# Kernel optimization log

Hardware: AMD Instinct MI355X
Metric: run time of the kernel (lower is better)

## Reference

```python
import jax, jax.numpy as jnp
import numpy as np

C = 32          # in_channels = out_channels = groups
K = 3           # kernel_size
STRIDE = 2
PAD = 1
DIL = 1
EPS = 1e-20


def _depthwise_convT(x, w):
    """Equivalent of torch.F.conv_transpose2d(x, w, groups=C, stride=STRIDE,
    padding=PAD, dilation=DIL) with w of shape (C, 1, K, K).
    Implemented as an lhs-dilated conv with a spatially flipped kernel."""
    w_f = w[:, :, ::-1, ::-1]
    pad = DIL * (K - 1) - PAD  # = 1 for K=3, PAD=1, DIL=1
    return jax.lax.conv_general_dilated(
        x, w_f,
        window_strides=(1, 1),
        padding=[(pad, pad), (pad, pad)],
        lhs_dilation=(STRIDE, STRIDE),
        rhs_dilation=(DIL, DIL),
        dimension_numbers=('NCHW', 'OIHW', 'NCHW'),
        feature_group_count=C)


def setup_inputs() -> dict:
    key = jax.random.key(0)
    k = jax.random.split(key, 7)
    B, H, W = 2, 176, 608
    # depths/confidences are positive (rand); gy is signed (randn)
    d = jax.random.uniform(k[0], (B, C, H, W), dtype=jnp.float32) + 0.5
    cd = jax.random.uniform(k[1], (B, C, H, W), dtype=jnp.float32)
    gy = jax.random.normal(k[2], (B, C, H, W), dtype=jnp.float32)
    cgy = jax.random.uniform(k[3], (B, C, H, W), dtype=jnp.float32)
    w_prop_raw = jax.random.normal(k[4], (1, C, 1, 1), dtype=jnp.float32)
    spatial_weight_raw = jax.random.normal(k[5], (C, 1, K, K), dtype=jnp.float32)
    bias = 0.01 * jax.random.normal(k[6], (1, C, 1, 1), dtype=jnp.float32)
    return {"d": d, "cd": cd, "gy": gy, "cgy": cgy,
            "w_prop_raw": w_prop_raw,
            "spatial_weight_raw": spatial_weight_raw,
            "bias": bias}


def reference(d, cd, gy, cgy, w_prop_raw, spatial_weight_raw, bias):
    # EnforcePos('softplus') on both learned weights
    w_prop = jax.nn.softplus(w_prop_raw)          # (1, C, 1, 1)
    sw = jax.nn.softplus(spatial_weight_raw)      # (C, 1, K, K)

    # roll-based vertical neighbor gather with edge confidence zeroing
    d_up = jnp.roll(d, 1, axis=2)
    cd_up = jnp.roll(cd, 1, axis=2).at[:, :, 0, :].set(0.0)
    d_down = jnp.roll(d, -1, axis=2)
    cd_down = jnp.roll(cd, -1, axis=2).at[:, :, -1, :].set(0.0)

    cgy_from_ds = cd_up * cd_up
    height = (cd_up * d_up + cd_down * d_down) / (cd_up + cd_down)
    gy_from_ds = (d_down - d_up) / 2.0 / height

    gy_f = (w_prop * cgy * gy + cgy_from_ds * gy_from_ds) / (w_prop * cgy + cgy_from_ds)
    cgy_f = (w_prop * cgy + cgy_from_ds) / (w_prop + 1.0)

    nom = _depthwise_convT(cgy_f * gy_f, sw)
    denom = _depthwise_convT(cgy_f, sw)
    cdenom = _depthwise_convT(jnp.ones_like(cgy_f), sw)

    # original adds bias twice: once unconditionally, once under use_bias
    gy_out = nom / (denom + EPS) + bias + bias
    cgy_out = denom / (cdenom + EPS)
    return gy_out / STRIDE, cgy_out
```

## Files before the change

kernel.cpp:

```cpp
#include <hip/hip_runtime.h>
#include <math.h>

#define B_   2
#define C_   32
#define H_   176
#define W_   608
#define HO_  351
#define WO_  1215
#define PLANE_O (HO_ * WO_)
#define OUT1_O  (B_ * C_ * PLANE_O)
#define EPS_ 1e-20f
#define NTH  512
#define W4   (W_ / 4)
#define HW_  304

typedef float f4_t __attribute__((ext_vector_type(4)));
typedef float f2_t __attribute__((ext_vector_type(2)));

__device__ __forceinline__ float softplus_f(float x) {
    return fmaxf(x, 0.0f) + log1pf(expf(-fabsf(x)));
}

extern "C" __global__ __launch_bounds__(NTH, 8)
void structn_rows(const float* __restrict__ d,
                  const float* __restrict__ cd,
                  const float* __restrict__ gy,
                  const float* __restrict__ cgy,
                  const float* __restrict__ wpr,
                  const float* __restrict__ swr,
                  const float* __restrict__ bias,
                  float* __restrict__ out)
{
    __shared__ float s_nE[5 * HW_];
    __shared__ float s_nO[5 * HW_];
    __shared__ float s_cE[5 * HW_];
    __shared__ float s_cO[5 * HW_];

    const int g     = blockIdx.x;
    const int plane = blockIdx.y;
    const int c     = plane & (C_ - 1);

    float sw[9];
#pragma unroll
    for (int k = 0; k < 9; ++k) sw[k] = softplus_f(swr[c * 9 + k]);
    const float wp      = softplus_f(wpr[c]);
    const float inv_wp1 = 1.0f / (wp + 1.0f);
    const float bv      = bias[c];
    const float icd_ee  = 1.0f / (sw[4] + EPS_);
    const float icd_eo  = 1.0f / (sw[3] + sw[5] + EPS_);
    const float icd_oe  = 1.0f / (sw[1] + sw[7] + EPS_);
    const float icd_oo  = 1.0f / (sw[0] + sw[2] + sw[6] + sw[8] + EPS_);

    const int r0  = g * 4;
    const int nrf = (r0 + 4 <= H_ - 1) ? 5 : (H_ - r0);

    const int pbase = plane * (H_ * W_);
    const float* __restrict__ dP  = d   + pbase;
    const float* __restrict__ cdP = cd  + pbase;
    const float* __restrict__ gyP = gy  + pbase;
    const float* __restrict__ cgP = cgy + pbase;

    const int ntask = nrf * W4;
    for (int idx = threadIdx.x; idx < ntask; idx += NTH) {
        const int rf = idx / W4;
        const int iw = (idx - rf * W4) << 2;
        const int iy = r0 + rf;
        const int up = (iy == 0)      ? (H_ - 1) : iy - 1;
        const int dn = (iy == H_ - 1) ? 0        : iy + 1;
        const float mu = (iy > 0)      ? 1.0f : 0.0f;
        const float md = (iy < H_ - 1) ? 1.0f : 0.0f;

        const f4_t du = *(const f4_t*)(dP  + up * W_ + iw);
        const f4_t dd = *(const f4_t*)(dP  + dn * W_ + iw);
        const f4_t cu = *(const f4_t*)(cdP + up * W_ + iw);
        const f4_t cn = *(const f4_t*)(cdP + dn * W_ + iw);
        const f4_t gg = *(const f4_t*)(gyP + iy * W_ + iw);
        const f4_t cg = *(const f4_t*)(cgP + iy * W_ + iw);

        f4_t sn4, sc4;
#pragma unroll
        for (int e = 0; e < 4; ++e) {
            const float cuv = cu[e] * mu;
            const float cnv = cn[e] * md;
            const float cfd = cuv * cuv;
            const float rs  = __builtin_amdgcn_rcpf(fmaf(cuv, du[e], cnv * dd[e]));
            const float gfd = 0.5f * (dd[e] - du[e]) * (cuv + cnv) * rs;
            const float num = fmaf(wp * cg[e], gg[e], cfd * gfd);
            const float den = fmaf(wp, cg[e], cfd);
            sn4[e] = num * inv_wp1;
            sc4[e] = den * inv_wp1;
        }
        const int eo = rf * HW_ + (iw >> 1);
        f2_t v;
        v[0] = sn4[0]; v[1] = sn4[2];  *(f2_t*)(s_nE + eo) = v;
        v[0] = sn4[1]; v[1] = sn4[3];  *(f2_t*)(s_nO + eo) = v;
        v[0] = sc4[0]; v[1] = sc4[2];  *(f2_t*)(s_cE + eo) = v;
        v[0] = sc4[1]; v[1] = sc4[3];  *(f2_t*)(s_cO + eo) = v;
    }
    __syncthreads();

    const int w    = threadIdx.x >> 6;
    const int lane = threadIdx.x & 63;
    const int oy   = g * 8 + w;
    if (oy >= HO_) return;

    const int p   = w & 1;
    const int lrA = w >> 1;

    const int ro0 = plane * PLANE_O + oy * WO_;
    float* __restrict__ o0 = out + ro0;
    float* __restrict__ o1 = out + OUT1_O + ro0;

    const int h  = (4 - (ro0 & 3)) & 3;
    const int n4 = (WO_ - h) >> 2;
    const int q  = h & 1;
    const int r  = (h >> 1) & 1;

    const float icdC = p ? icd_oe : icd_ee;
    const float icdO = p ? icd_oo : icd_eo;
    const float i0 = q ? icdO : icdC;
    const float i1 = q ? icdC : icdO;

    const float* __restrict__ nAE = s_nE + lrA * HW_;
    const float* __restrict__ nAO = s_nO + lrA * HW_;
    const float* __restrict__ cAE = s_cE + lrA * HW_;
    const float* __restrict__ cAO = s_cO + lrA * HW_;

#define VAL(E, O, j) (((j) & 1) ? (O)[((j) - 1) >> 1] : (E)[(j) >> 1])

    if (p == 0) {
        if (lane < 3) {
            const int ox = (lane < h) ? lane : (h + (n4 << 2) + lane - h);
            float den, nom, icd;
            if ((ox & 1) == 0) {
                const int j = ox >> 1;
                den = VAL(cAE, cAO, j) * sw[4];
                nom = VAL(nAE, nAO, j) * sw[4];
                icd = icd_ee;
            } else {
                const int j = (ox - 1) >> 1;
                den = VAL(cAE, cAO, j) * sw[5] + VAL(cAE, cAO, j + 1) * sw[3];
                nom = VAL(nAE, nAO, j) * sw[5] + VAL(nAE, nAO, j + 1) * sw[3];
                icd = icd_eo;
            }
            o0[ox] = fmaf(0.5f * nom, __builtin_amdgcn_rcpf(den + EPS_), bv);
            o1[ox] = den * icd;
        }
        const float* pa0 = r ? nAO : nAE;
        const float* pa1 = r ? nAE + 1 : nAO;
        const float* pa2 = r ? nAO + 1 : nAE + 1;
        const float* px0 = r ? cAO : cAE;
        const float* px1 = r ? cAE + 1 : cAO;
        const float* px2 = r ? cAO + 1 : cAE + 1;

        for (int k = lane; k < n4; k += 64) {
            const float a0 = pa0[k], a1 = pa1[k], a2 = pa2[k];
            const float x0 = px0[k], x1 = px1[k], x2 = px2[k];
            const float dC0 = x0 * sw[4], dC1 = x1 * sw[4], dC2 = x2 * sw[4];
            const float nC0 = a0 * sw[4], nC1 = a1 * sw[4], nC2 = a2 * sw[4];
            const float dF0 = x0 * sw[5] + x1 * sw[3];
            const float dF1 = x1 * sw[5] + x2 * sw[3];
            const float nF0 = a0 * sw[5] + a1 * sw[3];
            const float nF1 = a1 * sw[5] + a2 * sw[3];

            const float d0 = q ? dF0 : dC0, n0 = q ? nF0 : nC0;
            const float d1 = q ? dC1 : dF0, n1 = q ? nC1 : nF0;
            const float d2 = q ? dF1 : dC1, n2 = q ? nF1 : nC1;
            const float d3 = q ? dC2 : dF1, n3 = q ? nC2 : nF1;

            f4_t gv, qv;
            gv[0] = fmaf(0.5f * n0, __builtin_amdgcn_rcpf(d0 + EPS_), bv);
            gv[1] = fmaf(0.5f * n1, __builtin_amdgcn_rcpf(d1 + EPS_), bv);
            gv[2] = fmaf(0.5f * n2, __builtin_amdgcn_rcpf(d2 + EPS_), bv);
            gv[3] = fmaf(0.5f * n3, __builtin_amdgcn_rcpf(d3 + EPS_), bv);
            qv[0] = d0 * i0; qv[1] = d1 * i1; qv[2] = d2 * i0; qv[3] = d3 * i1;

            const int c0 = h + (k << 2);
            __builtin_nontemporal_store(gv, (f4_t*)(o0 + c0));
            __builtin_nontemporal_store(qv, (f4_t*)(o1 + c0));
        }
    } else {
        const float* __restrict__ nBE = nAE + HW_;
        const float* __restrict__ nBO = nAO + HW_;
        const float* __restrict__ cBE = cAE + HW_;
        const float* __restrict__ cBO = cAO + HW_;

        if (lane < 3) {
            const int ox = (lane < h) ? lane : (h + (n4 << 2) + lane - h);
            float den, nom, icd;
            if ((ox & 1) == 0) {
                const int j = ox >> 1;
                den = VAL(cAE, cAO, j) * sw[7] + VAL(cBE, cBO, j) * sw[1];
                nom = VAL(nAE, nAO, j) * sw[7] + VAL(nBE, nBO, j) * sw[1];
                icd = icd_oe;
            } else {
                const int j = (ox - 1) >> 1;
                den = VAL(cAE, cAO, j) * sw[8] + VAL(cAE, cAO, j + 1) * sw[6]
                    + VAL(cBE, cBO, j) * sw[2] + VAL(cBE, cBO, j + 1) * sw[0];
                nom = VAL(nAE, nAO, j) * sw[8] + VAL(nAE, nAO, j + 1) * sw[6]
                    + VAL(nBE, nBO, j) * sw[2] + VAL(nBE, nBO, j + 1) * sw[0];
                icd = icd_oo;
            }
            o0[ox] = fmaf(0.5f * nom, __builtin_amdgcn_rcpf(den + EPS_), bv);
            o1[ox] = den * icd;
        }

        const float* pa0 = r ? nAO : nAE;
        const float* pa1 = r ? nAE + 1 : nAO;
        const float* pa2 = r ? nAO + 1 : nAE + 1;
        const float* px0 = r ? cAO : cAE;
        const float* px1 = r ? cAE + 1 : cAO;
        const float* px2 = r ? cAO + 1 : cAE + 1;
        const float* pb0 = r ? nBO : nBE;
        const float* pb1 = r ? nBE + 1 : nBO;
        const float* pb2 = r ? nBO + 1 : nBE + 1;
        const float* py0 = r ? cBO : cBE;
        const float* py1 = r ? cBE + 1 : cBO;
        const float* py2 = r ? cBO + 1 : cBE + 1;

        for (int k = lane; k < n4; k += 64) {
            const float a0 = pa0[k], a1 = pa1[k], a2 = pa2[k];
            const float x0 = px0[k], x1 = px1[k], x2 = px2[k];
            const float b0 = pb0[k], b1 = pb1[k], b2 = pb2[k];
            const float y0 = py0[k], y1 = py1[k], y2 = py2[k];

            const float dC0 = x0 * sw[7] + y0 * sw[1];
            const float dC1 = x1 * sw[7] + y1 * sw[1];
            const float dC2 = x2 * sw[7] + y2 * sw[1];
            const float nC0 = a0 * sw[7] + b0 * sw[1];
            const float nC1 = a1 * sw[7] + b1 * sw[1];
            const float nC2 = a2 * sw[7] + b2 * sw[1];
            const float dF0 = x0 * sw[8] + x1 * sw[6] + y0 * sw[2] + y1 * sw[0];
            const float dF1 = x1 * sw[8] + x2 * sw[6] + y1 * sw[2] + y2 * sw[0];
            const float nF0 = a0 * sw[8] + a1 * sw[6] + b0 * sw[2] + b1 * sw[0];
            const float nF1 = a1 * sw[8] + a2 * sw[6] + b1 * sw[2] + b2 * sw[0];

            const float d0 = q ? dF0 : dC0, n0 = q ? nF0 : nC0;
            const float d1 = q ? dC1 : dF0, n1 = q ? nC1 : nF0;
            const float d2 = q ? dF1 : dC1, n2 = q ? nF1 : nC1;
            const float d3 = q ? dC2 : dF1, n3 = q ? nC2 : nF1;

            f4_t gv, qv;
            gv[0] = fmaf(0.5f * n0, __builtin_amdgcn_rcpf(d0 + EPS_), bv);
            gv[1] = fmaf(0.5f * n1, __builtin_amdgcn_rcpf(d1 + EPS_), bv);
            gv[2] = fmaf(0.5f * n2, __builtin_amdgcn_rcpf(d2 + EPS_), bv);
            gv[3] = fmaf(0.5f * n3, __builtin_amdgcn_rcpf(d3 + EPS_), bv);
            qv[0] = d0 * i0; qv[1] = d1 * i1; qv[2] = d2 * i0; qv[3] = d3 * i1;

            const int c0 = h + (k << 2);
            __builtin_nontemporal_store(gv, (f4_t*)(o0 + c0));
            __builtin_nontemporal_store(qv, (f4_t*)(o1 + c0));
        }
    }
#undef VAL
}

extern "C" void kernel_launch(void* const* d_in, const int* in_sizes, int n_in,
                              void* d_out, int out_size, void* d_ws, size_t ws_size,
                              hipStream_t stream) {
    const float* d    = (const float*)d_in[0];
    const float* cd   = (const float*)d_in[1];
    const float* gy   = (const float*)d_in[2];
    const float* cgy  = (const float*)d_in[3];
    const float* wpr  = (const float*)d_in[4];
    const float* swr  = (const float*)d_in[5];
    const float* bias = (const float*)d_in[6];
    float* out = (float*)d_out;

    dim3 grid(44, B_ * C_);
    structn_rows<<<grid, NTH, 0, stream>>>(d, cd, gy, cgy, wpr, swr, bias, out);
}
```

Measured before the change: 73.81 us.

## Process two row-groups per block, overlapping second staging with first output half

Each block now covers 16 output rows (8 input rows plus halo) instead of 8, with shared memory sized for 9 input rows. Staging of rows 5..8 is issued before the first half of outputs is computed, so global loads can overlap LDS reads and stores, and the shared halo row is loaded once instead of twice. The grid is halved and the occupancy hint drops from 8 to 6 blocks because of the larger LDS footprint, which cuts available parallelism.

```diff
diff --git a/kernel.cpp b/kernel.cpp
--- a/kernel.cpp
+++ b/kernel.cpp
@@ -13,6 +13,7 @@
 #define NTH  512
 #define W4   (W_ / 4)
 #define HW_  304
+#define NRLDS 9
 
 typedef float f4_t __attribute__((ext_vector_type(4)));
 typedef float f2_t __attribute__((ext_vector_type(2)));
@@ -21,8 +22,8 @@
     return fmaxf(x, 0.0f) + log1pf(expf(-fabsf(x)));
 }
 
-extern "C" __global__ __launch_bounds__(NTH, 8)
-void structn_rows(const float* __restrict__ d,
+extern "C" __global__ __launch_bounds__(NTH, 6)
+void structn_pipe(const float* __restrict__ d,
                   const float* __restrict__ cd,
                   const float* __restrict__ gy,
                   const float* __restrict__ cgy,
@@ -31,12 +32,12 @@
                   const float* __restrict__ bias,
                   float* __restrict__ out)
 {
-    __shared__ float s_nE[5 * HW_];
-    __shared__ float s_nO[5 * HW_];
-    __shared__ float s_cE[5 * HW_];
-    __shared__ float s_cO[5 * HW_];
-
-    const int g     = blockIdx.x;
+    __shared__ float s_nE[NRLDS * HW_];
+    __shared__ float s_nO[NRLDS * HW_];
+    __shared__ float s_cE[NRLDS * HW_];
+    __shared__ float s_cO[NRLDS * HW_];
+
+    const int G     = blockIdx.x;
     const int plane = blockIdx.y;
     const int c     = plane & (C_ - 1);
 
@@ -51,8 +52,7 @@
     const float icd_oe  = 1.0f / (sw[1] + sw[7] + EPS_);
     const float icd_oo  = 1.0f / (sw[0] + sw[2] + sw[6] + sw[8] + EPS_);
 
-    const int r0  = g * 4;
-    const int nrf = (r0 + 4 <= H_ - 1) ? 5 : (H_ - r0);
+    const int f0 = G * 8;
 
     const int pbase = plane * (H_ * W_);
     const float* __restrict__ dP  = d   + pbase;
@@ -60,199 +60,209 @@
     const float* __restrict__ gyP = gy  + pbase;
     const float* __restrict__ cgP = cgy + pbase;
 
-    const int ntask = nrf * W4;
-    for (int idx = threadIdx.x; idx < ntask; idx += NTH) {
-        const int rf = idx / W4;
-        const int iw = (idx - rf * W4) << 2;
-        const int iy = r0 + rf;
-        const int up = (iy == 0)      ? (H_ - 1) : iy - 1;
-        const int dn = (iy == H_ - 1) ? 0        : iy + 1;
-        const float mu = (iy > 0)      ? 1.0f : 0.0f;
-        const float md = (iy < H_ - 1) ? 1.0f : 0.0f;
-
-        const f4_t du = *(const f4_t*)(dP  + up * W_ + iw);
-        const f4_t dd = *(const f4_t*)(dP  + dn * W_ + iw);
-        const f4_t cu = *(const f4_t*)(cdP + up * W_ + iw);
-        const f4_t cn = *(const f4_t*)(cdP + dn * W_ + iw);
-        const f4_t gg = *(const f4_t*)(gyP + iy * W_ + iw);
-        const f4_t cg = *(const f4_t*)(cgP + iy * W_ + iw);
-
-        f4_t sn4, sc4;
+    auto stage_rows = [&](int j0, int j1) {
+        const int ntask = (j1 - j0) * W4;
+        for (int idx = threadIdx.x; idx < ntask; idx += NTH) {
+            const int rf = j0 + idx / W4;
+            const int iw = (idx - (rf - j0) * W4) << 2;
+            const int iy = f0 + rf;
+            const int up = (iy == 0)      ? (H_ - 1) : iy - 1;
+            const int dn = (iy == H_ - 1) ? 0        : iy + 1;
+            const float mu = (iy > 0)      ? 1.0f : 0.0f;
+            const float md = (iy < H_ - 1) ? 1.0f : 0.0f;
+
+            const f4_t du = *(const f4_t*)(dP  + up * W_ + iw);
+            const f4_t dd = *(const f4_t*)(dP  + dn * W_ + iw);
+            const f4_t cu = *(const f4_t*)(cdP + up * W_ + iw);
+            const f4_t cn = *(const f4_t*)(cdP + dn * W_ + iw);
+            const f4_t gg = *(const f4_t*)(gyP + iy * W_ + iw);
+            const f4_t cg = *(const f4_t*)(cgP + iy * W_ + iw);
+
+            f4_t sn4, sc4;
 #pragma unroll
-        for (int e = 0; e < 4; ++e) {
-            const float cuv = cu[e] * mu;
-            const float cnv = cn[e] * md;
-            const float cfd = cuv * cuv;
-            const float rs  = __builtin_amdgcn_rcpf(fmaf(cuv, du[e], cnv * dd[e]));
-            const float gfd = 0.5f * (dd[e] - du[e]) * (cuv + cnv) * rs;
-            const float num = fmaf(wp * cg[e], gg[e], cfd * gfd);
-            const float den = fmaf(wp, cg[e], cfd);
-            sn4[e] = num * inv_wp1;
-            sc4[e] = den * inv_wp1;
+            for (int e = 0; e < 4; ++e) {
+                const float cuv = cu[e] * mu;
+                const float cnv = cn[e] * md;
+                const float cfd = cuv * cuv;
+                const float rs  = __builtin_amdgcn_rcpf(fmaf(cuv, du[e], cnv * dd[e]));
+                const float gfd = 0.5f * (dd[e] - du[e]) * (cuv + cnv) * rs;
+                const float num = fmaf(wp * cg[e], gg[e], cfd * gfd);
+                const float den = fmaf(wp, cg[e], cfd);
+                sn4[e] = num * inv_wp1;
+                sc4[e] = den * inv_wp1;
+            }
+            const int eo = rf * HW_ + (iw >> 1);
+            f2_t v;
+            v[0] = sn4[0]; v[1] = sn4[2];  *(f2_t*)(s_nE + eo) = v;
+            v[0] = sn4[1]; v[1] = sn4[3];  *(f2_t*)(s_nO + eo) = v;
+            v[0] = sc4[0]; v[1] = sc4[2];  *(f2_t*)(s_cE + eo) = v;
+            v[0] = sc4[1]; v[1] = sc4[3];  *(f2_t*)(s_cO + eo) = v;
         }
-        const int eo = rf * HW_ + (iw >> 1);
-        f2_t v;
-        v[0] = sn4[0]; v[1] = sn4[2];  *(f2_t*)(s_nE + eo) = v;
-        v[0] = sn4[1]; v[1] = sn4[3];  *(f2_t*)(s_nO + eo) = v;
-        v[0] = sc4[0]; v[1] = sc4[2];  *(f2_t*)(s_cE + eo) = v;
-        v[0] = sc4[1]; v[1] = sc4[3];  *(f2_t*)(s_cO + eo) = v;
-    }
-    __syncthreads();
+    };
 
     const int w    = threadIdx.x >> 6;
     const int lane = threadIdx.x & 63;
-    const int oy   = g * 8 + w;
-    if (oy >= HO_) return;
-
-    const int p   = w & 1;
-    const int lrA = w >> 1;
-
-    const int ro0 = plane * PLANE_O + oy * WO_;
-    float* __restrict__ o0 = out + ro0;
-    float* __restrict__ o1 = out + OUT1_O + ro0;
-
-    const int h  = (4 - (ro0 & 3)) & 3;
-    const int n4 = (WO_ - h) >> 2;
-    const int q  = h & 1;
-    const int r  = (h >> 1) & 1;
-
-    const float icdC = p ? icd_oe : icd_ee;
-    const float icdO = p ? icd_oo : icd_eo;
-    const float i0 = q ? icdO : icdC;
-    const float i1 = q ? icdC : icdO;
-
-    const float* __restrict__ nAE = s_nE + lrA * HW_;
-    const float* __restrict__ nAO = s_nO + lrA * HW_;
-    const float* __restrict__ cAE = s_cE + lrA * HW_;
-    const float* __restrict__ cAO = s_cO + lrA * HW_;
+
+    auto consume_half = [&](int h) {
+        const int oy = G * 16 + 8 * h + w;
+        if (oy >= HO_) return;
+
+        const int p   = w & 1;
+        const int lrA = 4 * h + (w >> 1);
+
+        const int ro0 = plane * PLANE_O + oy * WO_;
+        float* __restrict__ o0 = out + ro0;
+        float* __restrict__ o1 = out + OUT1_O + ro0;
+
+        const int h4 = (4 - (ro0 & 3)) & 3;
+        const int n4 = (WO_ - h4) >> 2;
+        const int q  = h4 & 1;
+        const int r  = (h4 >> 1) & 1;
+
+        const float icdC = p ? icd_oe : icd_ee;
+        const float icdO = p ? icd_oo : icd_eo;
+        const float i0 = q ? icdO : icdC;
+        const float i1 = q ? icdC : icdO;
+
+        const float* __restrict__ nAE = s_nE + lrA * HW_;
+        const float* __restrict__ nAO = s_nO + lrA * HW_;
+        const float* __restrict__ cAE = s_cE + lrA * HW_;
+        const float* __restrict__ cAO = s_cO + lrA * HW_;
 
 #define VAL(E, O, j) (((j) & 1) ? (O)[((j) - 1) >> 1] : (E)[(j) >> 1])
-
-    if (p == 0) {
-        if (lane < 3) {
-            const int ox = (lane < h) ? lane : (h + (n4 << 2) + lane - h);
-            float den, nom, icd;
-            if ((ox & 1) == 0) {
-                const int j = ox >> 1;
-                den = VAL(cAE, cAO, j) * sw[4];
-                nom = VAL(nAE, nAO, j) * sw[4];
-                icd = icd_ee;
-            } else {
-                const int j = (ox - 1) >> 1;
-                den = VAL(cAE, cAO, j) * sw[5] + VAL(cAE, cAO, j + 1) * sw[3];
-                nom = VAL(nAE, nAO, j) * sw[5] + VAL(nAE, nAO, j + 1) * sw[3];
-                icd = icd_eo;
-            }
-            o0[ox] = fmaf(0.5f * nom, __builtin_amdgcn_rcpf(den + EPS_), bv);
-            o1[ox] = den * icd;
+        if (p == 0) {
+            if (lane < 3) {
+                const int ox = (lane < h4) ? lane : (h4 + (n4 << 2) + lane - h4);
+                float den, nom, icd;
+                if ((ox & 1) == 0) {
+                    const int j = ox >> 1;
+                    den = VAL(cAE, cAO, j) * sw[4];
+                    nom = VAL(nAE, nAO, j) * sw[4];
+                    icd = icd_ee;
+                } else {
+                    const int j = (ox - 1) >> 1;
+                    den = VAL(cAE, cAO, j) * sw[5] + VAL(cAE, cAO, j + 1) * sw[3];
+                    nom = VAL(nAE, nAO, j) * sw[5] + VAL(nAE, nAO, j + 1) * sw[3];
+                    icd = icd_eo;
+                }
+                o0[ox] = fmaf(0.5f * nom, __builtin_amdgcn_rcpf(den + EPS_), bv);
+                o1[ox] = den * icd;
+            }
+            const float* pa0 = r ? nAO : nAE;
+            const float* pa1 = r ? nAE + 1 : nAO;
+            const float* pa2 = r ? nAO + 1 : nAE + 1;
+            const float* px0 = r ? cAO : cAE;
+            const float* px1 = r ? cAE + 1 : cAO;
+            const float* px2 = r ? cAO + 1 : cAE + 1;
+
+            for (int k = lane; k < n4; k += 64) {
+                const float a0 = pa0[k], a1 = pa1[k], a2 = pa2[k];
+                const float x0 = px0[k], x1 = px1[k], x2 = px2[k];
+                const float dC0 = x0 * sw[4], dC1 = x1 * sw[4], dC2 = x2 * sw[4];
+                const float nC0 = a0 * sw[4], nC1 = a1 * sw[4], nC2 = a2 * sw[4];
+                const float dF0 = x0 * sw[5] + x1 * sw[3];
+                const float dF1 = x1 * sw[5] + x2 * sw[3];
+                const float nF0 = a0 * sw[5] + a1 * sw[3];
+                const float nF1 = a1 * sw[5] + a2 * sw[3];
+
+                const float d0 = q ? dF0 : dC0, n0 = q ? nF0 : nC0;
+                const float d1 = q ? dC1 : dF0, n1 = q ? nC1 : nF0;
+                const float d2 = q ? dF1 : dC1, n2 = q ? nF1 : nC1;
+                const float d3 = q ? dC2 : dF1, n3 = q ? nC2 : nF1;
+
+                f4_t gv, qv;
+                gv[0] = fmaf(0.5f * n0, __builtin_amdgcn_rcpf(d0 + EPS_), bv);
+                gv[1] = fmaf(0.5f * n1, __builtin_amdgcn_rcpf(d1 + EPS_), bv);
+                gv[2] = fmaf(0.5f * n2, __builtin_amdgcn_rcpf(d2 + EPS_), bv);
+                gv[3] = fmaf(0.5f * n3, __builtin_amdgcn_rcpf(d3 + EPS_), bv);
+                qv[0] = d0 * i0; qv[1] = d1 * i1; qv[2] = d2 * i0; qv[3] = d3 * i1;
+
+                const int c0 = h4 + (k << 2);
+                __builtin_nontemporal_store(gv, (f4_t*)(o0 + c0));
+                __builtin_nontemporal_store(qv, (f4_t*)(o1 + c0));
+            }
+        } else {
+            const float* __restrict__ nBE = nAE + HW_;
+            const float* __restrict__ nBO = nAO + HW_;
+            const float* __restrict__ cBE = cAE + HW_;
+            const float* __restrict__ cBO = cAO + HW_;
+
+            if (lane < 3) {
+                const int ox = (lane < h4) ? lane : (h4 + (n4 << 2) + lane - h4);
+                float den, nom, icd;
+                if ((ox & 1) == 0) {
+                    const int j = ox >> 1;
+                    den = VAL(cAE, cAO, j) * sw[7] + VAL(cBE, cBO, j) * sw[1];
+                    nom = VAL(nAE, nAO, j) * sw[7] + VAL(nBE, nBO, j) * sw[1];
+                    icd = icd_oe;
+                } else {
+                    const int j = (ox - 1) >> 1;
+                    den = VAL(cAE, cAO, j) * sw[8] + VAL(cAE, cAO, j + 1) * sw[6]
+                        + VAL(cBE, cBO, j) * sw[2] + VAL(cBE, cBO, j + 1) * sw[0];
+                    nom = VAL(nAE, nAO, j) * sw[8] + VAL(nAE, nAO, j + 1) * sw[6]
+                        + VAL(nBE, nBO, j) * sw[2] + VAL(nBE, nBO, j + 1) * sw[0];
+                    icd = icd_oo;
+                }
+                o0[ox] = fmaf(0.5f * nom, __builtin_amdgcn_rcpf(den + EPS_), bv);
+                o1[ox] = den * icd;
+            }
+
+            const float* pa0 = r ? nAO : nAE;
+            const float* pa1 = r ? nAE + 1 : nAO;
+            const float* pa2 = r ? nAO + 1 : nAE + 1;
+            const float* px0 = r ? cAO : cAE;
+            const float* px1 = r ? cAE + 1 : cAO;
+            const float* px2 = r ? cAO + 1 : cAE + 1;
+            const float* pb0 = r ? nBO : nBE;
+            const float* pb1 = r ? nBE + 1 : nBO;
+            const float* pb2 = r ? nBO + 1 : nBE + 1;
+            const float* py0 = r ? cBO : cBE;
+            const float* py1 = r ? cBE + 1 : cBO;
+            const float* py2 = r ? cBO + 1 : cBE + 1;
+
+            for (int k = lane; k < n4; k += 64) {
+                const float a0 = pa0[k], a1 = pa1[k], a2 = pa2[k];
+                const float x0 = px0[k], x1 = px1[k], x2 = px2[k];
+                const float b0 = pb0[k], b1 = pb1[k], b2 = pb2[k];
+                const float y0 = py0[k], y1 = py1[k], y2 = py2[k];
+
+                const float dC0 = x0 * sw[7] + y0 * sw[1];
+                const float dC1 = x1 * sw[7] + y1 * sw[1];
+                const float dC2 = x2 * sw[7] + y2 * sw[1];
+                const float nC0 = a0 * sw[7] + b0 * sw[1];
+                const float nC1 = a1 * sw[7] + b1 * sw[1];
+                const float nC2 = a2 * sw[7] + b2 * sw[1];
+                const float dF0 = x0 * sw[8] + x1 * sw[6] + y0 * sw[2] + y1 * sw[0];
+                const float dF1 = x1 * sw[8] + x2 * sw[6] + y1 * sw[2] + y2 * sw[0];
+                const float nF0 = a0 * sw[8] + a1 * sw[6] + b0 * sw[2] + b1 * sw[0];
+                const float nF1 = a1 * sw[8] + a2 * sw[6] + b1 * sw[2] + b2 * sw[0];
+
+                const float d0 = q ? dF0 : dC0, n0 = q ? nF0 : nC0;
+                const float d1 = q ? dC1 : dF0, n1 = q ? nC1 : nF0;
+                const float d2 = q ? dF1 : dC1, n2 = q ? nF1 : nC1;
+                const float d3 = q ? dC2 : dF1, n3 = q ? nC2 : nF1;
+
+                f4_t gv, qv;
+                gv[0] = fmaf(0.5f * n0, __builtin_amdgcn_rcpf(d0 + EPS_), bv);
+                gv[1] = fmaf(0.5f * n1, __builtin_amdgcn_rcpf(d1 + EPS_), bv);
+                gv[2] = fmaf(0.5f * n2, __builtin_amdgcn_rcpf(d2 + EPS_), bv);
+                gv[3] = fmaf(0.5f * n3, __builtin_amdgcn_rcpf(d3 + EPS_), bv);
+                qv[0] = d0 * i0; qv[1] = d1 * i1; qv[2] = d2 * i0; qv[3] = d3 * i1;
+
+                const int c0 = h4 + (k << 2);
+                __builtin_nontemporal_store(gv, (f4_t*)(o0 + c0));
+                __builtin_nontemporal_store(qv, (f4_t*)(o1 + c0));
+            }
         }
-        const float* pa0 = r ? nAO : nAE;
-        const float* pa1 = r ? nAE + 1 : nAO;
-        const float* pa2 = r ? nAO + 1 : nAE + 1;
-        const float* px0 = r ? cAO : cAE;
-        const float* px1 = r ? cAE + 1 : cAO;
-        const float* px2 = r ? cAO + 1 : cAE + 1;
-
-        for (int k = lane; k < n4; k += 64) {
-            const float a0 = pa0[k], a1 = pa1[k], a2 = pa2[k];
-            const float x0 = px0[k], x1 = px1[k], x2 = px2[k];
-            const float dC0 = x0 * sw[4], dC1 = x1 * sw[4], dC2 = x2 * sw[4];
-            const float nC0 = a0 * sw[4], nC1 = a1 * sw[4], nC2 = a2 * sw[4];
-            const float dF0 = x0 * sw[5] + x1 * sw[3];
-            const float dF1 = x1 * sw[5] + x2 * sw[3];
-            const float nF0 = a0 * sw[5] + a1 * sw[3];
-            const float nF1 = a1 * sw[5] + a2 * sw[3];
-
-            const float d0 = q ? dF0 : dC0, n0 = q ? nF0 : nC0;
-            const float d1 = q ? dC1 : dF0, n1 = q ? nC1 : nF0;
-            const float d2 = q ? dF1 : dC1, n2 = q ? nF1 : nC1;
-            const float d3 = q ? dC2 : dF1, n3 = q ? nC2 : nF1;
-
-            f4_t gv, qv;
-            gv[0] = fmaf(0.5f * n0, __builtin_amdgcn_rcpf(d0 + EPS_), bv);
-            gv[1] = fmaf(0.5f * n1, __builtin_amdgcn_rcpf(d1 + EPS_), bv);
-            gv[2] = fmaf(0.5f * n2, __builtin_amdgcn_rcpf(d2 + EPS_), bv);
-            gv[3] = fmaf(0.5f * n3, __builtin_amdgcn_rcpf(d3 + EPS_), bv);
-            qv[0] = d0 * i0; qv[1] = d1 * i1; qv[2] = d2 * i0; qv[3] = d3 * i1;
-
-            const int c0 = h + (k << 2);
-            __builtin_nontemporal_store(gv, (f4_t*)(o0 + c0));
-            __builtin_nontemporal_store(qv, (f4_t*)(o1 + c0));
-        }
-    } else {
-        const float* __restrict__ nBE = nAE + HW_;
-        const float* __restrict__ nBO = nAO + HW_;
-        const float* __restrict__ cBE = cAE + HW_;
-        const float* __restrict__ cBO = cAO + HW_;
-
-        if (lane < 3) {
-            const int ox = (lane < h) ? lane : (h + (n4 << 2) + lane - h);
-            float den, nom, icd;
-            if ((ox & 1) == 0) {
-                const int j = ox >> 1;
-                den = VAL(cAE, cAO, j) * sw[7] + VAL(cBE, cBO, j) * sw[1];
-                nom = VAL(nAE, nAO, j) * sw[7] + VAL(nBE, nBO, j) * sw[1];
-                icd = icd_oe;
-            } else {
-                const int j = (ox - 1) >> 1;
-                den = VAL(cAE, cAO, j) * sw[8] + VAL(cAE, cAO, j + 1) * sw[6]
-                    + VAL(cBE, cBO, j) * sw[2] + VAL(cBE, cBO, j + 1) * sw[0];
-                nom = VAL(nAE, nAO, j) * sw[8] + VAL(nAE, nAO, j + 1) * sw[6]
-                    + VAL(nBE, nBO, j) * sw[2] + VAL(nBE, nBO, j + 1) * sw[0];
-                icd = icd_oo;
-            }
-            o0[ox] = fmaf(0.5f * nom, __builtin_amdgcn_rcpf(den + EPS_), bv);
-            o1[ox] = den * icd;
-        }
-
-        const float* pa0 = r ? nAO : nAE;
-        const float* pa1 = r ? nAE + 1 : nAO;
-        const float* pa2 = r ? nAO + 1 : nAE + 1;
-        const float* px0 = r ? cAO : cAE;
-        const float* px1 = r ? cAE + 1 : cAO;
-        const float* px2 = r ? cAO + 1 : cAE + 1;
-        const float* pb0 = r ? nBO : nBE;
-        const float* pb1 = r ? nBE + 1 : nBO;
-        const float* pb2 = r ? nBO + 1 : nBE + 1;
-        const float* py0 = r ? cBO : cBE;
-        const float* py1 = r ? cBE + 1 : cBO;
-        const float* py2 = r ? cBO + 1 : cBE + 1;
-
-        for (int k = lane; k < n4; k += 64) {
-            const float a0 = pa0[k], a1 = pa1[k], a2 = pa2[k];
-            const float x0 = px0[k], x1 = px1[k], x2 = px2[k];
-            const float b0 = pb0[k], b1 = pb1[k], b2 = pb2[k];
-            const float y0 = py0[k], y1 = py1[k], y2 = py2[k];
-
-            const float dC0 = x0 * sw[7] + y0 * sw[1];
-            const float dC1 = x1 * sw[7] + y1 * sw[1];
-            const float dC2 = x2 * sw[7] + y2 * sw[1];
-            const float nC0 = a0 * sw[7] + b0 * sw[1];
-            const float nC1 = a1 * sw[7] + b1 * sw[1];
-            const float nC2 = a2 * sw[7] + b2 * sw[1];
-            const float dF0 = x0 * sw[8] + x1 * sw[6] + y0 * sw[2] + y1 * sw[0];
-            const float dF1 = x1 * sw[8] + x2 * sw[6] + y1 * sw[2] + y2 * sw[0];
-            const float nF0 = a0 * sw[8] + a1 * sw[6] + b0 * sw[2] + b1 * sw[0];
-            const float nF1 = a1 * sw[8] + a2 * sw[6] + b1 * sw[2] + b2 * sw[0];
-
-            const float d0 = q ? dF0 : dC0, n0 = q ? nF0 : nC0;
-            const float d1 = q ? dC1 : dF0, n1 = q ? nC1 : nF0;
-            const float d2 = q ? dF1 : dC1, n2 = q ? nF1 : nC1;
-            const float d3 = q ? dC2 : dF1, n3 = q ? nC2 : nF1;
-
-            f4_t gv, qv;
-            gv[0] = fmaf(0.5f * n0, __builtin_amdgcn_rcpf(d0 + EPS_), bv);
-            gv[1] = fmaf(0.5f * n1, __builtin_amdgcn_rcpf(d1 + EPS_), bv);
-            gv[2] = fmaf(0.5f * n2, __builtin_amdgcn_rcpf(d2 + EPS_), bv);
-            gv[3] = fmaf(0.5f * n3, __builtin_amdgcn_rcpf(d3 + EPS_), bv);
-            qv[0] = d0 * i0; qv[1] = d1 * i1; qv[2] = d2 * i0; qv[3] = d3 * i1;
-
-            const int c0 = h + (k << 2);
-            __builtin_nontemporal_store(gv, (f4_t*)(o0 + c0));
-            __builtin_nontemporal_store(qv, (f4_t*)(o1 + c0));
-        }
-    }
 #undef VAL
+    };
+
+    stage_rows(0, 5);
+    __syncthreads();
+    stage_rows(5, min(NRLDS, H_ - f0));
+    consume_half(0);
+    __syncthreads();
+    consume_half(1);
 }
 
 extern "C" void kernel_launch(void* const* d_in, const int* in_sizes, int n_in,
@@ -267,6 +277,6 @@
     const float* bias = (const float*)d_in[6];
     float* out = (float*)d_out;
 
-    dim3 grid(44, B_ * C_);
-    structn_rows<<<grid, NTH, 0, stream>>>(d, cd, gy, cgy, wpr, swr, bias, out);
+    dim3 grid(22, B_ * C_);
+    structn_pipe<<<grid, NTH, 0, stream>>>(d, cd, gy, cgy, wpr, swr, bias, out);
 }
```

Result: faster. 68.70 us (median of 2 runs) (-6.9%).
